# Kernel optimization log

Hardware: AMD Instinct MI355X
Metric: run time of the kernel (lower is better)

The kernel has to match this reference:

```python
import jax, jax.numpy as jnp
import numpy as np

N = 117000   # vocab / number of WordNet synsets (square adjacency)
E = 500000   # number of COO edges
B, T = 4, 64 # batch, seq len


def setup_inputs() -> dict:
    key = jax.random.key(0)
    k1, k2, k3, k4 = jax.random.split(key, 4)
    logits = jax.random.normal(k1, (B, T, N), dtype=jnp.float32)
    # ensure every row index appears at least once so row-normalization never divides by zero
    row = jnp.concatenate([jnp.arange(N, dtype=jnp.int32),
                           jax.random.randint(k2, (E - N,), 0, N, dtype=jnp.int32)])
    col = jax.random.randint(k3, (E,), 0, N, dtype=jnp.int32)
    edge_index = jnp.stack([row, col], axis=0)  # [2, E]
    vv = jax.random.uniform(k4, (E,), dtype=jnp.float32, minval=0.1, maxval=1.0)
    return {"logits": logits, "vv": vv, "edge_index": edge_index}


def reference(logits, vv, edge_index):
    # StructuredLogits.forward with DEHARDCODE_ALPHA=1.0, renormalize=True:
    #   neighbors = spmm(A, logits_flat^T)^T ; neighbors /= row_sum ; out = neighbors + logits
    row, col = edge_index[0], edge_index[1]
    n = logits.shape[-1]
    x = logits.reshape(-1, n).T                              # [N, BT]
    contrib = vv[:, None] * x[col]                           # [E, BT] gather + scale
    neigh_T = jax.ops.segment_sum(contrib, row, num_segments=n)   # [N, BT] scatter-add (SpMM)
    row_sum = jax.ops.segment_sum(vv, row, num_segments=n)        # [N] row-normalizer
    neighbors = (neigh_T / row_sum[:, None]).T.reshape(logits.shape)
    return neighbors + logits
```

## Files before the change

kernel.cpp:

```cpp
#include <hip/hip_runtime.h>
#include <hip/hip_fp16.h>

#define NN 117000
#define BT 256

#define SCAN_CHUNK 1024
#define SCAN_NB ((NN + SCAN_CHUNK - 1) / SCAN_CHUNK)
#define SCAN_P2_T 128

#define ROWS_PB 32
#define LDS_STRIDE 257

union U8 { uint2 u; __half2 h[2]; };


__global__ void hist_kernel(const int* __restrict__ row, int* __restrict__ count, int E) {
    int e = blockIdx.x * blockDim.x + threadIdx.x;
    if (e < E) atomicAdd(&count[row[e]], 1);
}

__global__ void scan_phase1(const int* __restrict__ count, int* __restrict__ block_sums) {
    __shared__ int s[256];
    int base = blockIdx.x * SCAN_CHUNK + threadIdx.x * 4;
    int sum = 0;
#pragma unroll
    for (int j = 0; j < 4; ++j) {
        int idx = base + j;
        if (idx < NN) sum += count[idx];
    }
    s[threadIdx.x] = sum;
    __syncthreads();
    for (int off = 128; off > 0; off >>= 1) {
        if (threadIdx.x < off) s[threadIdx.x] += s[threadIdx.x + off];
        __syncthreads();
    }
    if (threadIdx.x == 0) block_sums[blockIdx.x] = s[0];
}

__global__ void scan_phase2(int* __restrict__ block_sums, int* __restrict__ row_ptr) {
    __shared__ int s[SCAN_P2_T];
    int t = threadIdx.x;
    int v = (t < SCAN_NB) ? block_sums[t] : 0;
    s[t] = v;
    __syncthreads();
    for (int off = 1; off < SCAN_P2_T; off <<= 1) {
        int u = (t >= off) ? s[t - off] : 0;
        __syncthreads();
        s[t] += u;
        __syncthreads();
    }
    if (t < SCAN_NB) block_sums[t] = (t == 0) ? 0 : s[t - 1];
    if (t == SCAN_P2_T - 1) row_ptr[NN] = s[SCAN_NB - 1];
}

__global__ void scan_phase3(int* __restrict__ row_ptr, const int* __restrict__ block_offs,
                            int* __restrict__ cursor) {
    __shared__ int s[256];
    int base = blockIdx.x * SCAN_CHUNK + threadIdx.x * 4;
    int v[4];
    int sum = 0;
#pragma unroll
    for (int j = 0; j < 4; ++j) {
        int idx = base + j;
        v[j] = (idx < NN) ? row_ptr[idx] : 0;
        sum += v[j];
    }
    s[threadIdx.x] = sum;
    __syncthreads();
    for (int off = 1; off < 256; off <<= 1) {
        int u = (threadIdx.x >= off) ? s[threadIdx.x - off] : 0;
        __syncthreads();
        s[threadIdx.x] += u;
        __syncthreads();
    }
    int prefix = block_offs[blockIdx.x] + ((threadIdx.x == 0) ? 0 : s[threadIdx.x - 1]);
#pragma unroll
    for (int j = 0; j < 4; ++j) {
        int idx = base + j;
        if (idx < NN) {
            row_ptr[idx] = prefix;
            cursor[idx]  = prefix;
            prefix += v[j];
        }
    }
}

__global__ void scatter_kernel(const int* __restrict__ row, const int* __restrict__ col,
                               const float* __restrict__ vv, int* __restrict__ cursor,
                               int2* __restrict__ edge_s, int E) {
    int e = blockIdx.x * blockDim.x + threadIdx.x;
    if (e >= E) return;
    int p = atomicAdd(&cursor[row[e]], 1);
    edge_s[p] = make_int2(col[e], __float_as_int(vv[e]));
}


__global__ void transpose_h_kernel(const float* __restrict__ logits, __half* __restrict__ xT) {
    __shared__ float s[64][33];
    int tx = threadIdx.x & 31;
    int ty = threadIdx.x >> 5;
    int i0  = blockIdx.x * 32;
    int bt0 = blockIdx.y * 64;
    int i = i0 + tx;
    if (i < NN) {
#pragma unroll
        for (int r = 0; r < 8; ++r) {
            int bt = bt0 + ty + r * 8;
            s[ty + r * 8][tx] = logits[(size_t)bt * NN + i];
        }
    }
    __syncthreads();
#pragma unroll
    for (int r = 0; r < 4; ++r) {
        int il = ty + r * 8;
        int i2 = i0 + il;
        if (i2 < NN) {
            __half2 h = __floats2half2_rn(s[2 * tx][il], s[2 * tx + 1][il]);
            ((__half2*)(xT + (size_t)i2 * BT + bt0))[tx] = h;
        }
    }
}

__global__ void row_gather_fused_kernel(const int* __restrict__ row_ptr,
                                        const int2* __restrict__ edge_s,
                                        const __half* __restrict__ xT,
                                        const float* __restrict__ logits,
                                        float* __restrict__ out) {
    __shared__ float s[ROWS_PB][LDS_STRIDE];
    int wave = threadIdx.x >> 6;
    int lane = threadIdx.x & 63;
    int i0 = blockIdx.x * ROWS_PB;
    int iw = i0 + wave * 4;
    const uint2* xT2 = (const uint2*)xT;

    if (iw < NN) {
        int rp = 0;
        if (lane < 5) {
            int idx = iw + lane;
            if (idx > NN) idx = NN;
            rp = row_ptr[idx];
        }
        int kw0 = __shfl(rp, 0);
        int b0  = __shfl(rp, 1);
        int b1  = __shfl(rp, 2);
        int b2  = __shfl(rp, 3);
        int b3  = __shfl(rp, 4);
        int kw1 = b3;

        float4 acc = make_float4(0.f, 0.f, 0.f, 0.f);
        float rs = 0.f;
        int r_cur = 0;
        int next_b = b0;

#define FINALIZE_ROW() do {                                                   \
            float inv = (rs > 0.f) ? (1.0f / rs) : 0.f;                       \
            int rl = (wave << 2) + r_cur;                                     \
            s[rl][0 * 64 + lane] = acc.x * inv;                               \
            s[rl][1 * 64 + lane] = acc.y * inv;                               \
            s[rl][2 * 64 + lane] = acc.z * inv;                               \
            s[rl][3 * 64 + lane] = acc.w * inv;                               \
            acc = make_float4(0.f, 0.f, 0.f, 0.f);                            \
            rs = 0.f;                                                         \
            ++r_cur;                                                          \
            next_b = (r_cur == 1) ? b1 : ((r_cur == 2) ? b2 : b3);            \
        } while (0)

        while (r_cur < 4 && next_b == kw0) FINALIZE_ROW();

        for (int kb = kw0; kb < kw1; kb += 64) {
            int nk = min(64, kw1 - kb);
            int2 ed = make_int2(0, 0);
            if (lane < nk) ed = edge_s[kb + lane];
            int   ccol = ed.x;
            float cval = __int_as_float(ed.y);

            uint2 p0 = make_uint2(0u, 0u), p1 = p0, p2 = p0, p3 = p0;
#define ISSUE(dst, jj) do {                                                   \
                if ((jj) < nk) {                                              \
                    int cn = __shfl(ccol, (jj));                              \
                    dst = xT2[(size_t)cn * (BT / 4) + lane];                  \
                }                                                             \
            } while (0)
            ISSUE(p0, 0); ISSUE(p1, 1); ISSUE(p2, 2); ISSUE(p3, 3);

#define CONSUME(pp, jj) do {                                                  \
                if ((jj) < nk) {                                              \
                    float v = __shfl(cval, (jj));                             \
                    rs += v;                                                  \
                    U8 t; t.u = pp;                                           \
                    float2 fa = __half22float2(t.h[0]);                       \
                    float2 fb = __half22float2(t.h[1]);                       \
                    acc.x += v * fa.x; acc.y += v * fa.y;                     \
                    acc.z += v * fb.x; acc.w += v * fb.y;                     \
                    int kg = kb + (jj) + 1;                                   \
                    while (r_cur < 4 && kg == next_b) FINALIZE_ROW();         \
                }                                                             \
            } while (0)

            for (int j = 0; j < nk; j += 4) {
                uint2 q0 = make_uint2(0u, 0u), q1 = q0, q2 = q0, q3 = q0;
                ISSUE(q0, j + 4); ISSUE(q1, j + 5); ISSUE(q2, j + 6); ISSUE(q3, j + 7);
                CONSUME(p0, j + 0);
                CONSUME(p1, j + 1);
                CONSUME(p2, j + 2);
                CONSUME(p3, j + 3);
                p0 = q0; p1 = q1; p2 = q2; p3 = q3;
            }
#undef ISSUE
#undef CONSUME
        }
#undef FINALIZE_ROW
    }
    __syncthreads();

    int tx = threadIdx.x & 31;
    int ty = threadIdx.x >> 5;
    int i = i0 + tx;
    if (i < NN) {
#pragma unroll
        for (int r = 0; r < 16; ++r) {
            int bt = r * 16 + ty;
            int c = ((bt & 3) << 6) + (bt >> 2);
            size_t idx = (size_t)bt * NN + i;
            out[idx] = logits[idx] + s[tx][c];
        }
    }
}


__global__ void transpose_kernel(const float* __restrict__ logits, float* __restrict__ xT) {
    __shared__ float s[32][33];
    int tx = threadIdx.x & 31;
    int ty = threadIdx.x >> 5;
    int i0  = blockIdx.x * 32;
    int bt0 = blockIdx.y * 32;
    int i = i0 + tx;
#pragma unroll
    for (int r = 0; r < 4; ++r) {
        int bt = bt0 + ty + r * 8;
        if (i < NN) s[ty + r * 8][tx] = logits[(size_t)bt * NN + i];
    }
    __syncthreads();
#pragma unroll
    for (int r = 0; r < 4; ++r) {
        int i2 = i0 + ty + r * 8;
        if (i2 < NN) xT[(size_t)i2 * BT + bt0 + tx] = s[tx][ty + r * 8];
    }
}

__global__ void rowsum_kernel(const int* __restrict__ row, const float* __restrict__ vv,
                              float* __restrict__ row_sum, int E) {
    int e = blockIdx.x * blockDim.x + threadIdx.x;
    if (e < E) atomicAdd(&row_sum[row[e]], vv[e]);
}

__global__ void edge_kernel(const int* __restrict__ row, const int* __restrict__ col,
                            const float* __restrict__ vv, const float* __restrict__ xT,
                            float* __restrict__ acc, int E) {
    int e = blockIdx.x * 4 + (threadIdx.x >> 6);
    if (e >= E) return;
    int lane = threadIdx.x & 63;
    int r = row[e];
    int c = col[e];
    float v = vv[e];
    float4 x4 = ((const float4*)(xT + (size_t)c * BT))[lane];
    float* dst = acc + (size_t)r * BT + lane * 4;
    atomicAdd(dst + 0, v * x4.x);
    atomicAdd(dst + 1, v * x4.y);
    atomicAdd(dst + 2, v * x4.z);
    atomicAdd(dst + 3, v * x4.w);
}

__global__ void finalize_div_kernel(const float* __restrict__ logits, const float* __restrict__ acc,
                                    const float* __restrict__ row_sum, float* __restrict__ out) {
    __shared__ float s[32][33];
    __shared__ float rs[32];
    int tx = threadIdx.x & 31;
    int ty = threadIdx.x >> 5;
    int i0  = blockIdx.x * 32;
    int bt0 = blockIdx.y * 32;
#pragma unroll
    for (int r = 0; r < 4; ++r) {
        int il = ty + r * 8;
        int i = i0 + il;
        if (i < NN) s[il][tx] = acc[(size_t)i * BT + bt0 + tx];
    }
    if (threadIdx.x < 32) {
        int i = i0 + (int)threadIdx.x;
        rs[threadIdx.x] = (i < NN) ? row_sum[i] : 1.0f;
    }
    __syncthreads();
#pragma unroll
    for (int r = 0; r < 4; ++r) {
        int bt = bt0 + ty + r * 8;
        int i = i0 + tx;
        if (i < NN) {
            size_t idx = (size_t)bt * NN + i;
            out[idx] = logits[idx] + s[tx][ty + r * 8] / rs[tx];
        }
    }
}

extern "C" void kernel_launch(void* const* d_in, const int* in_sizes, int n_in,
                              void* d_out, int out_size, void* d_ws, size_t ws_size,
                              hipStream_t stream) {
    const float* logits = (const float*)d_in[0];
    const float* vv     = (const float*)d_in[1];
    const int*   ei     = (const int*)d_in[2];
    const int E = in_sizes[1];
    const int* row = ei;
    const int* col = ei + E;
    float* out = (float*)d_out;

    const size_t accN = (size_t)NN * BT;

    const int e_blocks = (E + 255) / 256;

    const size_t need_csr = (size_t)E * sizeof(int2)
                          + accN * sizeof(__half)
                          + (size_t)(NN + 1 + NN + SCAN_NB) * sizeof(int);

    if (ws_size >= need_csr) {
        int2*   edge_s     = (int2*)d_ws;
        __half* xT         = (__half*)(edge_s + E);
        int*    row_ptr    = (int*)(xT + accN);
        int*    cursor     = row_ptr + (NN + 1);
        int*    block_sums = cursor + NN;

        dim3 tgrid((NN + 31) / 32, BT / 64);
        const int fuse_blocks = (NN + ROWS_PB - 1) / ROWS_PB;

        hipMemsetAsync(row_ptr, 0, (NN + 1) * sizeof(int), stream);
        hist_kernel<<<e_blocks, 256, 0, stream>>>(row, row_ptr, E);
        scan_phase1<<<SCAN_NB, 256, 0, stream>>>(row_ptr, block_sums);
        scan_phase2<<<1, SCAN_P2_T, 0, stream>>>(block_sums, row_ptr);
        scan_phase3<<<SCAN_NB, 256, 0, stream>>>(row_ptr, block_sums, cursor);
        scatter_kernel<<<e_blocks, 256, 0, stream>>>(row, col, vv, cursor, edge_s, E);
        transpose_h_kernel<<<tgrid, 256, 0, stream>>>(logits, xT);
        row_gather_fused_kernel<<<fuse_blocks, 512, 0, stream>>>(row_ptr, edge_s, xT,
                                                                 logits, out);
    } else {
        float* acc     = (float*)d_ws;
        float* xT      = acc + accN;
        float* row_sum = xT + accN;
        dim3 tgrid32((NN + 31) / 32, BT / 32);
        hipMemsetAsync(acc, 0, accN * sizeof(float), stream);
        hipMemsetAsync(row_sum, 0, NN * sizeof(float), stream);
        rowsum_kernel<<<e_blocks, 256, 0, stream>>>(row, vv, row_sum, E);
        transpose_kernel<<<tgrid32, 256, 0, stream>>>(logits, xT);
        edge_kernel<<<(E + 3) / 4, 256, 0, stream>>>(row, col, vv, xT, acc, E);
        finalize_div_kernel<<<tgrid32, 256, 0, stream>>>(logits, acc, row_sum, out);
    }
}
```

Measured before the change: 367.8 us.

## Deepen gather prefetch to 12 in-flight loads with readlane broadcasts

Reworks the SpMM gather loop so 12 row loads are in flight per wave instead of 4, refilling each slot right after it is consumed rather than in batches of four. Wave-uniform column and value broadcasts now use readlane instead of shfl, which avoids LDS-based permute traffic. Adds launch bounds of 512 threads with a minimum of 8 blocks to steer register allocation. The deeper prefetch is meant to hide gather latency, but it uses more registers and may spill or lower occupancy.

New measurement: 365.5 us. No clear change (-0.6%).

```diff
diff --git a/kernel.cpp b/kernel.cpp
--- a/kernel.cpp
+++ b/kernel.cpp
@@ -12,6 +12,10 @@
 #define LDS_STRIDE 257
 
 union U8 { uint2 u; __half2 h[2]; };
+
+__device__ inline float readlane_f(float x, int l) {
+    return __int_as_float(__builtin_amdgcn_readlane(__float_as_int(x), l));
+}
 
 
 __global__ void hist_kernel(const int* __restrict__ row, int* __restrict__ count, int E) {
@@ -121,11 +125,12 @@
     }
 }
 
-__global__ void row_gather_fused_kernel(const int* __restrict__ row_ptr,
-                                        const int2* __restrict__ edge_s,
-                                        const __half* __restrict__ xT,
-                                        const float* __restrict__ logits,
-                                        float* __restrict__ out) {
+__global__ void __launch_bounds__(512, 8)
+row_gather_fused_kernel(const int* __restrict__ row_ptr,
+                        const int2* __restrict__ edge_s,
+                        const __half* __restrict__ xT,
+                        const float* __restrict__ logits,
+                        float* __restrict__ out) {
     __shared__ float s[ROWS_PB][LDS_STRIDE];
     int wave = threadIdx.x >> 6;
     int lane = threadIdx.x & 63;
@@ -174,18 +179,18 @@
             int   ccol = ed.x;
             float cval = __int_as_float(ed.y);
 
-            uint2 p0 = make_uint2(0u, 0u), p1 = p0, p2 = p0, p3 = p0;
+            uint2 p0, p1, p2, p3, p4, p5, p6, p7, p8, p9, p10, p11;
+            p0 = p1 = p2 = p3 = p4 = p5 = p6 = p7 = p8 = p9 = p10 = p11
+               = make_uint2(0u, 0u);
 #define ISSUE(dst, jj) do {                                                   \
                 if ((jj) < nk) {                                              \
-                    int cn = __shfl(ccol, (jj));                              \
+                    int cn = __builtin_amdgcn_readlane(ccol, (jj));           \
                     dst = xT2[(size_t)cn * (BT / 4) + lane];                  \
                 }                                                             \
             } while (0)
-            ISSUE(p0, 0); ISSUE(p1, 1); ISSUE(p2, 2); ISSUE(p3, 3);
-
 #define CONSUME(pp, jj) do {                                                  \
                 if ((jj) < nk) {                                              \
-                    float v = __shfl(cval, (jj));                             \
+                    float v = readlane_f(cval, (jj));                         \
                     rs += v;                                                  \
                     U8 t; t.u = pp;                                           \
                     float2 fa = __half22float2(t.h[0]);                       \
@@ -197,14 +202,23 @@
                 }                                                             \
             } while (0)
 
-            for (int j = 0; j < nk; j += 4) {
-                uint2 q0 = make_uint2(0u, 0u), q1 = q0, q2 = q0, q3 = q0;
-                ISSUE(q0, j + 4); ISSUE(q1, j + 5); ISSUE(q2, j + 6); ISSUE(q3, j + 7);
-                CONSUME(p0, j + 0);
-                CONSUME(p1, j + 1);
-                CONSUME(p2, j + 2);
-                CONSUME(p3, j + 3);
-                p0 = q0; p1 = q1; p2 = q2; p3 = q3;
+            ISSUE(p0, 0);  ISSUE(p1, 1);  ISSUE(p2, 2);  ISSUE(p3, 3);
+            ISSUE(p4, 4);  ISSUE(p5, 5);  ISSUE(p6, 6);  ISSUE(p7, 7);
+            ISSUE(p8, 8);  ISSUE(p9, 9);  ISSUE(p10, 10); ISSUE(p11, 11);
+
+            for (int j = 0; j < nk; j += 12) {
+                CONSUME(p0,  j + 0);  ISSUE(p0,  j + 12);
+                CONSUME(p1,  j + 1);  ISSUE(p1,  j + 13);
+                CONSUME(p2,  j + 2);  ISSUE(p2,  j + 14);
+                CONSUME(p3,  j + 3);  ISSUE(p3,  j + 15);
+                CONSUME(p4,  j + 4);  ISSUE(p4,  j + 16);
+                CONSUME(p5,  j + 5);  ISSUE(p5,  j + 17);
+                CONSUME(p6,  j + 6);  ISSUE(p6,  j + 18);
+                CONSUME(p7,  j + 7);  ISSUE(p7,  j + 19);
+                CONSUME(p8,  j + 8);  ISSUE(p8,  j + 20);
+                CONSUME(p9,  j + 9);  ISSUE(p9,  j + 21);
+                CONSUME(p10, j + 10); ISSUE(p10, j + 22);
+                CONSUME(p11, j + 11); ISSUE(p11, j + 23);
             }
 #undef ISSUE
 #undef CONSUME
```
